# Kernel tuning notes

Hardware: AMD Instinct MI355X
Metric: run time of the kernel (lower is better)

## Reference

```python
import jax, jax.numpy as jnp
import numpy as np

EMBED = 256; G = 8; NC = 6; NL = 4; NP = 13
BS = 1; NA = 900
IMG_W, IMG_H = 704.0, 256.0
LEVEL_HW = [(64, 176), (32, 88), (16, 44), (8, 22)]


def setup_inputs() -> dict:
    key = jax.random.key(0)
    ks = jax.random.split(key, 12)
    inp = {}
    inp["instance_feature"] = jax.random.normal(ks[0], (BS, NA, EMBED), jnp.float32)
    inp["anchor_embed"] = jax.random.normal(ks[1], (BS, NA, EMBED), jnp.float32)
    # key points in normalized [0,1) cube; projection matrix maps them to pixel coords
    inp["key_points"] = jax.random.uniform(ks[2], (BS, NA, NP, 3), jnp.float32)
    for i, (h, w) in enumerate(LEVEL_HW):
        inp[f"fm{i}"] = jax.random.normal(ks[3 + i], (BS, NC, EMBED, h, w), jnp.float32)
    # intrinsics-like projection: x->x*W, y->y*H, depth ~ z+0.5, plus per-camera jitter
    base = jnp.array([[IMG_W, 0.0, 0.0, 0.0],
                      [0.0, IMG_H, 0.0, 0.0],
                      [0.0, 0.0, 1.0, 0.5],
                      [0.0, 0.0, 0.0, 1.0]], jnp.float32)
    inp["projection_mat"] = base[None, None] + 0.05 * jax.random.normal(ks[7], (BS, NC, 4, 4), jnp.float32)
    inp["image_wh"] = jnp.broadcast_to(jnp.array([IMG_W, IMG_H], jnp.float32), (BS, NC, 2))
    inp["w_weights"] = 0.02 * jax.random.normal(ks[8], (EMBED, G * NC * NL * NP), jnp.float32)
    inp["b_weights"] = jnp.zeros((G * NC * NL * NP,), jnp.float32)
    inp["w_out"] = 0.02 * jax.random.normal(ks[9], (EMBED, EMBED), jnp.float32)
    inp["b_out"] = jnp.zeros((EMBED,), jnp.float32)
    return inp


def _grid_sample(fm, grid):
    # fm: (B, C, H, W); grid: (B, A, P, 2) in [-1,1]. Bilinear, zero padding,
    # align_corners=False (torch F.grid_sample defaults). Returns (B, A, P, C).
    B, C, H, W = fm.shape
    A, P = grid.shape[1], grid.shape[2]
    gx = (grid[..., 0] + 1.0) * (W * 0.5) - 0.5
    gy = (grid[..., 1] + 1.0) * (H * 0.5) - 0.5
    x0 = jnp.floor(gx); y0 = jnp.floor(gy)
    fmf = jnp.transpose(fm.reshape(B, C, H * W), (0, 2, 1))  # (B, HW, C)

    def gather(xi, yi):
        valid = (xi >= 0) & (xi <= W - 1) & (yi >= 0) & (yi <= H - 1)
        xc = jnp.clip(xi, 0, W - 1).astype(jnp.int32)
        yc = jnp.clip(yi, 0, H - 1).astype(jnp.int32)
        idx = (yc * W + xc).reshape(B, A * P, 1)
        g = jnp.take_along_axis(fmf, idx, axis=1).reshape(B, A, P, C)
        return g * valid[..., None].astype(fm.dtype)

    wx1 = gx - x0; wx0 = 1.0 - wx1
    wy1 = gy - y0; wy0 = 1.0 - wy1
    return (gather(x0, y0) * (wx0 * wy0)[..., None]
            + gather(x0 + 1.0, y0) * (wx1 * wy0)[..., None]
            + gather(x0, y0 + 1.0) * (wx0 * wy1)[..., None]
            + gather(x0 + 1.0, y0 + 1.0) * (wx1 * wy1)[..., None])


def reference(instance_feature, anchor_embed, key_points, fm0, fm1, fm2, fm3,
              projection_mat, image_wh, w_weights, b_weights, w_out, b_out):
    bs, na = instance_feature.shape[:2]
    gd = EMBED // G
    # _get_weights: softmax over (cams*levels*pts) jointly, per group
    feat = instance_feature + anchor_embed
    w = (feat @ w_weights + b_weights).reshape(bs, na, NC * NL * NP, G)
    w = jax.nn.softmax(w, axis=2).reshape(bs, na, NC, NL, NP, G)
    # feature_sampling: project 3D key points to each camera's pixel plane
    kp_h = jnp.concatenate([key_points, jnp.ones_like(key_points[..., :1])], axis=-1)
    p2 = jnp.einsum('bcij,banj->bcani', projection_mat, kp_h)  # (bs,cams,na,pts,4)
    xy = p2[..., :2] / jnp.maximum(p2[..., 2:3], 1e-5)
    grid = (xy / image_wh[:, :, None, None]) * 2.0 - 1.0
    grid = grid.reshape(bs * NC, na, NP, 2)
    # bilinear sample every pyramid level for every camera
    feats = jnp.stack([
        _grid_sample(fm.reshape(bs * NC, EMBED, fm.shape[-2], fm.shape[-1]), grid)
        for fm in (fm0, fm1, fm2, fm3)
    ], axis=0)  # (L, bs*cams, na, pts, E)
    feats = feats.reshape(NL, bs, NC, na, NP, G, gd)
    # multi_view_level_fusion: weighted sum over cams and levels, per group
    fused = jnp.einsum('baclpg,lbcapgd->bapgd', w, feats).reshape(bs, na, NP, EMBED)
    out = fused.sum(axis=2)  # sum over key points
    return out @ w_out + b_out + instance_feature  # output_proj + residual 'add'
```

## Files before the change

kernel.cpp:

```cpp
#include <hip/hip_runtime.h>
#include <hip/hip_bf16.h>
#include <hip/hip_fp16.h>
#include <cstdint>

#define EMBED 256
#define GPS 8
#define NCAM 6
#define NLVL 4
#define NPT 13
#define NANC 900
#define NSAMP (NCAM*NLVL*NPT)
#define NWCOL (GPS*NSAMP)
#define MPAD 928
#define WSTRIDE 328
#define MAXENT 352

#define FMOFF0 0
#define FMOFF1 17301504
#define FMOFF2 21626880
#define FMOFF3 22708224
#define TALL_BYTES 22978560

typedef __attribute__((ext_vector_type(8))) short bf16x8;
typedef __attribute__((ext_vector_type(16))) float f32x16;
typedef __attribute__((ext_vector_type(2))) float v2f;

__device__ __forceinline__ ushort bf16bits(float x) {
    __hip_bfloat16 h = __float2bfloat16(x);
    return *reinterpret_cast<ushort*>(&h);
}

__global__ __launch_bounds__(256) void k_prep(
        const float* __restrict__ fm0, const float* __restrict__ fm1,
        const float* __restrict__ fm2, const float* __restrict__ fm3,
        unsigned char* __restrict__ t0, unsigned char* __restrict__ t1,
        unsigned char* __restrict__ t2, unsigned char* __restrict__ t3,
        const float* __restrict__ wlin, __hip_bfloat16* __restrict__ wt,
        const float* __restrict__ inst, const float* __restrict__ anch,
        __hip_bfloat16* __restrict__ featB,
        const float* __restrict__ kp, const float* __restrict__ proj,
        float* __restrict__ pxy) {
    __shared__ ushort lds2[128 * 64];
    int b = blockIdx.x;
    int t = threadIdx.x;
    if (b < 1404) {
        const float* in; unsigned char* outp; int HW, chunks, lb;
        if (b < 1056)      { in = fm0; outp = t0; HW = 11264; chunks = 176; lb = b; }
        else if (b < 1320) { in = fm1; outp = t1; HW = 2816;  chunks = 44;  lb = b - 1056; }
        else if (b < 1386) { in = fm2; outp = t2; HW = 704;   chunks = 11;  lb = b - 1320; }
        else               { in = fm3; outp = t3; HW = 176;   chunks = 3;   lb = b - 1386; }
        int c = lb / chunks;
        int hw0 = (lb - c * chunks) * 64;
        int q = t & 15, eg = t >> 4;
        bool vld = (hw0 + q * 4 + 3) < HW;
        const float* srcq = in + (size_t)c * EMBED * HW + hw0 + q * 4;
        float4 vals[16];
        #pragma unroll
        for (int r = 0; r < 16; r++) {
            int e = 2 * eg + (r & 1) + 32 * (r >> 1);
            vals[r] = vld ? *(const float4*)(srcq + (size_t)e * HW)
                          : make_float4(0.f, 0.f, 0.f, 0.f);
        }
        #pragma unroll
        for (int rp = 0; rp < 8; rp++) {
            int ep = eg + 16 * rp;
            int s2 = (ep >> 1) & 62;
            float4 va = vals[2 * rp], vb = vals[2 * rp + 1];
            uint p0 = (uint)__builtin_amdgcn_cvt_pk_fp8_f32(va.x, vb.x, 0, false) & 0xffff;
            uint p1 = (uint)__builtin_amdgcn_cvt_pk_fp8_f32(va.y, vb.y, 0, false) & 0xffff;
            uint p2 = (uint)__builtin_amdgcn_cvt_pk_fp8_f32(va.z, vb.z, 0, false) & 0xffff;
            uint p3 = (uint)__builtin_amdgcn_cvt_pk_fp8_f32(va.w, vb.w, 0, false) & 0xffff;
            int col01 = (q * 4) ^ s2;
            int col23 = (q * 4 + 2) ^ s2;
            *reinterpret_cast<uint*>(&lds2[ep * 64 + col01]) = p0 | (p1 << 16);
            *reinterpret_cast<uint*>(&lds2[ep * 64 + col23]) = p2 | (p3 << 16);
        }
        __syncthreads();
        ushort* outb = reinterpret_cast<ushort*>(outp) + ((size_t)c * HW + hw0) * 128;
        #pragma unroll
        for (int r = 0; r < 8; r++) {
            int flat = r * 2048 + t * 8;
            int hw = flat >> 8;
            int ep0 = (flat & 255) >> 1;
            if (hw0 + hw < HW) {
                ushort4 u;
                #pragma unroll
                for (int j = 0; j < 4; j++) {
                    int ep = ep0 + j;
                    int s2 = (ep >> 1) & 62;
                    u[j] = lds2[ep * 64 + (hw ^ s2)];
                }
                *reinterpret_cast<ushort4*>(outb + flat / 2) = u;
            }
        }
    } else if (b < 1560) {
        int b1 = b - 1404;
        int kt = b1 / 39, nt = b1 - kt * 39;
        int k0 = kt * 64, n0 = nt * 64;
        int grp = t >> 6, nn = t & 63;
        #pragma unroll
        for (int r = 0; r < 16; r++) {
            int kk = grp * 16 + r;
            lds2[kk * 65 + nn] = bf16bits(wlin[(size_t)(k0 + kk) * NWCOL + n0 + nn]);
        }
        __syncthreads();
        ushort* wtb = reinterpret_cast<ushort*>(wt);
        int kk2 = t & 63;
        #pragma unroll
        for (int r = 0; r < 16; r++) {
            int nn2 = grp * 16 + r;
            wtb[(size_t)(n0 + nn2) * EMBED + k0 + kk2] = lds2[kk2 * 65 + nn2];
        }
    } else if (b < 1785) {
        int base = (b - 1560) * 1024 + t * 4;
        float4 a = *(const float4*)&inst[base];
        float4 c = *(const float4*)&anch[base];
        ushort4 r;
        r.x = bf16bits(a.x + c.x); r.y = bf16bits(a.y + c.y);
        r.z = bf16bits(a.z + c.z); r.w = bf16bits(a.w + c.w);
        *reinterpret_cast<ushort4*>(reinterpret_cast<ushort*>(featB) + base) = r;
    } else if (b < 1792) {
        int base = 900 * EMBED + (b - 1785) * 1024 + t * 4;
        ushort4 z; z.x = z.y = z.z = z.w = 0;
        *reinterpret_cast<ushort4*>(reinterpret_cast<ushort*>(featB) + base) = z;
    } else {
        int i = (b - 1792) * 256 + t;
        if (i < NANC * NCAM * NPT) {
            int a = i / (NCAM * NPT);
            int r = i - a * (NCAM * NPT);
            int c = r / NPT;
            int p = r - c * NPT;
            const float* M = proj + c * 16;
            const float* k3 = kp + ((size_t)a * NPT + p) * 3;
            float kx = k3[0], ky = k3[1], kz = k3[2];
            float X = M[0] * kx + M[1] * ky + M[2] * kz + M[3];
            float Y = M[4] * kx + M[5] * ky + M[6] * kz + M[7];
            float Z = M[8] * kx + M[9] * ky + M[10] * kz + M[11];
            float invz = 1.f / fmaxf(Z, 1e-5f);
            pxy[(size_t)i * 2 + 0] = X * invz;
            pxy[(size_t)i * 2 + 1] = Y * invz;
        }
    }
}

#define MT 29
#define NT 78
__global__ __launch_bounds__(256) void k_gemm(const __hip_bfloat16* __restrict__ featB,
                                              const __hip_bfloat16* __restrict__ wt,
                                              const float* __restrict__ blin,
                                              float* __restrict__ logits) {
    int wv = threadIdx.x >> 6, lane = threadIdx.x & 63;
    int idx = blockIdx.x * 4 + wv;
    if (idx >= MT * NT) return;
    int mt = idx % MT, nt = idx / MT;
    int m0 = mt * 32, n0 = nt * 32;
    int l31 = lane & 31;
    int khalf = (lane >> 5) * 8;
    const short* ap = reinterpret_cast<const short*>(featB) + (size_t)(m0 + l31) * EMBED + khalf;
    const short* bp = reinterpret_cast<const short*>(wt)    + (size_t)(n0 + l31) * EMBED + khalf;
    f32x16 acc = {};
    #pragma unroll 8
    for (int ki = 0; ki < 16; ki++) {
        bf16x8 a = *reinterpret_cast<const bf16x8*>(ap + ki * 16);
        bf16x8 bb = *reinterpret_cast<const bf16x8*>(bp + ki * 16);
        acc = __builtin_amdgcn_mfma_f32_32x32x16_bf16(a, bb, acc, 0, 0, 0);
    }
    float bias = blin[n0 + l31];
    int colg = n0 + l31;
    #pragma unroll
    for (int r = 0; r < 16; r++) {
        int row = (r & 3) + 8 * (r >> 2) + 4 * (lane >> 5);
        int grow = m0 + row;
        if (grow < NANC)
            logits[(size_t)grow * NWCOL + colg] = acc[r] + bias;
    }
}

__global__ __launch_bounds__(512) void k_aggregate(const unsigned char* __restrict__ tAll,
                                                   const float* __restrict__ logits,
                                                   const float* __restrict__ pxy,
                                                   const float* __restrict__ wout,
                                                   const float* __restrict__ bout,
                                                   const float* __restrict__ inst,
                                                   float* __restrict__ out) {
    __shared__ float wT[GPS * WSTRIDE];
    __shared__ float xyS[NCAM * NPT * 2];
    __shared__ float redS[8][EMBED];
    __shared__ float pS[EMBED];
    __shared__ int4  eOff[MAXENT];
    __shared__ float4 eW[MAXENT];
    __shared__ int   eS[MAXENT];
    __shared__ int   cntS;
    int a = blockIdx.x;
    int tid = threadIdx.x;
    int wave = tid >> 6;
    int lane = tid & 63;
    if (tid == 0) cntS = 0;
    for (int j = tid; j < NWCOL; j += 512)
        wT[(j & 7) * WSTRIDE + (j >> 3)] = logits[(size_t)a * NWCOL + j];
    for (int j = tid; j < NCAM * NPT * 2; j += 512)
        xyS[j] = pxy[(size_t)a * NCAM * NPT * 2 + j];
    __syncthreads();
    {
        int g = wave;
        float m = -1e30f;
        for (int s = lane; s < NSAMP; s += 64) m = fmaxf(m, wT[g * WSTRIDE + s]);
        #pragma unroll
        for (int off = 32; off; off >>= 1) m = fmaxf(m, __shfl_xor(m, off));
        float ssum = 0.f;
        for (int s = lane; s < NSAMP; s += 64) ssum += __expf(wT[g * WSTRIDE + s] - m);
        #pragma unroll
        for (int off = 32; off; off >>= 1) ssum += __shfl_xor(ssum, off);
        float rs = 1.f / ssum;
        for (int s = lane; s < NSAMP; s += 64)
            wT[g * WSTRIDE + s] = __expf(wT[g * WSTRIDE + s] - m) * rs;
    }
    {
        bool valid = false; int4 o4; float4 w4;
        if (tid < NSAMP) {
            int c = tid / 52, rem = tid - c * 52;
            int l = rem / 13, p = rem - l * 13;
            float X = xyS[(c * NPT + p) * 2], Y = xyS[(c * NPT + p) * 2 + 1];
            int Wl = 176 >> l, Hl = 64 >> l;
            float scale = 0.25f / (float)(1 << l);
            float gx = fmaf(X, scale, -0.5f);
            float gy = fmaf(Y, scale, -0.5f);
            float x0f = floorf(gx), y0f = floorf(gy);
            float fx = gx - x0f, fy = gy - y0f;
            int x0 = (int)x0f, y0 = (int)y0f;
            int x1 = x0 + 1, y1 = y0 + 1;
            bool vx0 = (x0 >= 0) && (x0 < Wl);
            bool vx1 = (x1 >= 0) && (x1 < Wl);
            bool vy0 = (y0 >= 0) && (y0 < Hl);
            bool vy1 = (y1 >= 0) && (y1 < Hl);
            w4.x = (vx0 && vy0) ? (1.f - fx) * (1.f - fy) : 0.f;
            w4.y = (vx1 && vy0) ? fx * (1.f - fy) : 0.f;
            w4.z = (vx0 && vy1) ? (1.f - fx) * fy : 0.f;
            w4.w = (vx1 && vy1) ? fx * fy : 0.f;
            if (w4.x + w4.y + w4.z + w4.w > 0.f) {
                valid = true;
                int xc0 = min(max(x0, 0), Wl - 1), xc1 = min(max(x1, 0), Wl - 1);
                int yc0 = min(max(y0, 0), Hl - 1), yc1 = min(max(y1, 0), Hl - 1);
                const int lvlBase[4] = { FMOFF0, FMOFF1, FMOFF2, FMOFF3 };
                int cb = lvlBase[l] + c * (Wl * Hl) * EMBED;
                o4.x = cb + (yc0 * Wl + xc0) * EMBED;
                o4.y = cb + (yc0 * Wl + xc1) * EMBED;
                o4.z = cb + (yc1 * Wl + xc0) * EMBED;
                o4.w = cb + (yc1 * Wl + xc1) * EMBED;
            }
        }
        unsigned long long mask = __ballot(valid);
        int prefix = __popcll(mask & ((1ull << lane) - 1ull));
        int wcount = __popcll(mask);
        int basev = 0;
        if (lane == 0 && wcount) basev = atomicAdd(&cntS, wcount);
        basev = __shfl(basev, 0);
        if (valid) {
            int pos = basev + prefix;
            eOff[pos] = o4; eW[pos] = w4; eS[pos] = tid;
        }
    }
    __syncthreads();
    int cnt = cntS;
    int cnt_pad = (cnt + 15) & ~15;
    for (int j = cnt + tid; j < cnt_pad + 16; j += 512) {
        eOff[j] = make_int4(0, 0, 0, 0);
        eW[j] = make_float4(0.f, 0.f, 0.f, 0.f);
        eS[j] = 0;
    }
    __syncthreads();
    int e0 = lane * 4;
    int g = lane >> 3;
    float a0 = 0.f, a1 = 0.f, a2 = 0.f, a3 = 0.f;
    auto consume = [&](const float4& w, int sIdx,
                       uint c00, uint c01, uint c10, uint c11) {
        float wg = wT[g * WSTRIDE + sIdx];
        float wwx = wg * w.x, wwy = wg * w.y, wwz = wg * w.z, www = wg * w.w;
        v2f l00 = __builtin_amdgcn_cvt_pk_f32_fp8(c00, false);
        v2f h00 = __builtin_amdgcn_cvt_pk_f32_fp8(c00, true);
        v2f l01 = __builtin_amdgcn_cvt_pk_f32_fp8(c01, false);
        v2f h01 = __builtin_amdgcn_cvt_pk_f32_fp8(c01, true);
        v2f l10 = __builtin_amdgcn_cvt_pk_f32_fp8(c10, false);
        v2f h10 = __builtin_amdgcn_cvt_pk_f32_fp8(c10, true);
        v2f l11 = __builtin_amdgcn_cvt_pk_f32_fp8(c11, false);
        v2f h11 = __builtin_amdgcn_cvt_pk_f32_fp8(c11, true);
        a0 = fmaf(wwx, l00.x, fmaf(wwy, l01.x, fmaf(wwz, l10.x, fmaf(www, l11.x, a0))));
        a1 = fmaf(wwx, l00.y, fmaf(wwy, l01.y, fmaf(wwz, l10.y, fmaf(www, l11.y, a1))));
        a2 = fmaf(wwx, h00.x, fmaf(wwy, h01.x, fmaf(wwz, h10.x, fmaf(www, h11.x, a2))));
        a3 = fmaf(wwx, h00.y, fmaf(wwy, h01.y, fmaf(wwz, h10.y, fmaf(www, h11.y, a3))));
    };
    int per = cnt_pad >> 3;
    if (per > 0) {
        int idx = wave;
        int4 oA = eOff[idx]; float4 wA = eW[idx]; int sA = eS[idx];
        uint vA0 = *(const uint*)(tAll + oA.x + e0);
        uint vA1 = *(const uint*)(tAll + oA.y + e0);
        uint vA2 = *(const uint*)(tAll + oA.z + e0);
        uint vA3 = *(const uint*)(tAll + oA.w + e0);
        for (int it = 0; it < per; it += 2) {
            int j = idx + 8;
            int4 oB = eOff[j]; float4 wB = eW[j]; int sB = eS[j];
            uint vB0 = *(const uint*)(tAll + oB.x + e0);
            uint vB1 = *(const uint*)(tAll + oB.y + e0);
            uint vB2 = *(const uint*)(tAll + oB.z + e0);
            uint vB3 = *(const uint*)(tAll + oB.w + e0);
            consume(wA, sA, vA0, vA1, vA2, vA3);
            idx = j + 8;
            if (it + 2 < per) {
                oA = eOff[idx]; wA = eW[idx]; sA = eS[idx];
                vA0 = *(const uint*)(tAll + oA.x + e0);
                vA1 = *(const uint*)(tAll + oA.y + e0);
                vA2 = *(const uint*)(tAll + oA.z + e0);
                vA3 = *(const uint*)(tAll + oA.w + e0);
            }
            consume(wB, sB, vB0, vB1, vB2, vB3);
        }
    }
    redS[wave][e0 + 0] = a0; redS[wave][e0 + 1] = a1;
    redS[wave][e0 + 2] = a2; redS[wave][e0 + 3] = a3;
    __syncthreads();
    int col = tid & 255;
    int kh = tid >> 8;
    if (kh == 0) {
        float s = redS[0][col] + redS[1][col] + redS[2][col] + redS[3][col]
                + redS[4][col] + redS[5][col] + redS[6][col] + redS[7][col];
        redS[0][col] = s;
    }
    __syncthreads();
    float acc = 0.f;
    int kbase = kh * 128;
    #pragma unroll 8
    for (int k = 0; k < 128; k++)
        acc = fmaf(redS[0][kbase + k], wout[(size_t)(kbase + k) * EMBED + col], acc);
    if (kh == 1) pS[col] = acc;
    __syncthreads();
    if (kh == 0)
        out[(size_t)a * EMBED + col] = acc + pS[col] + bout[col] + inst[(size_t)a * EMBED + col];
}

extern "C" void kernel_launch(void* const* d_in, const int* in_sizes, int n_in,
                              void* d_out, int out_size, void* d_ws, size_t ws_size,
                              hipStream_t stream) {
    const float* inst = (const float*)d_in[0];
    const float* anch = (const float*)d_in[1];
    const float* kp   = (const float*)d_in[2];
    const float* fm0  = (const float*)d_in[3];
    const float* fm1  = (const float*)d_in[4];
    const float* fm2  = (const float*)d_in[5];
    const float* fm3  = (const float*)d_in[6];
    const float* proj = (const float*)d_in[7];
    const float* wlin = (const float*)d_in[9];
    const float* blin = (const float*)d_in[10];
    const float* wout = (const float*)d_in[11];
    const float* bout = (const float*)d_in[12];
    float* out = (float*)d_out;

    char* ws = (char*)d_ws;
    size_t off = 0;
    auto alloc = [&](size_t bytes) -> void* {
        void* p = ws + off;
        off = (off + bytes + 255) & ~(size_t)255;
        return p;
    };
    unsigned char* tAll = (unsigned char*)alloc((size_t)TALL_BYTES);
    unsigned char* t0 = tAll + FMOFF0;
    unsigned char* t1 = tAll + FMOFF1;
    unsigned char* t2 = tAll + FMOFF2;
    unsigned char* t3 = tAll + FMOFF3;
    __hip_bfloat16* wt    = (__hip_bfloat16*)alloc((size_t)NWCOL * EMBED * 2);
    __hip_bfloat16* featB = (__hip_bfloat16*)alloc((size_t)MPAD * EMBED * 2);
    float* logits = (float*)alloc((size_t)NANC * NWCOL * 4);
    float* pxy    = (float*)alloc((size_t)NANC * NCAM * NPT * 2 * 4);

    k_prep<<<dim3(2067), 256, 0, stream>>>(fm0, fm1, fm2, fm3, t0, t1, t2, t3,
                                           wlin, wt, inst, anch, featB, kp, proj, pxy);
    k_gemm<<<dim3((MT * NT + 3) / 4), 256, 0, stream>>>(featB, wt, blin, logits);
    k_aggregate<<<dim3(NANC), 512, 0, stream>>>(tAll, logits, pxy,
                                                wout, bout, inst, out);
}
```

Baseline: 194.9 us.

## Process two sample entries per wave with 8-byte gathers and defer softmax normalization

Each wave now splits into two 32-lane halves that handle different sample entries at the same time. Each lane gathers 8 fp8 channels with a uint2 load instead of 4, and the halves are combined with a cross-half shuffle before the block reduction. The softmax second exp pass is dropped by storing the unnormalized exponentials and applying the per-group reciprocal after the reduction. The aim is more memory-level parallelism per gather and fewer transcendental ops. In exchange each lane holds more accumulator registers, and entries are padded to a multiple of 32.

```diff
diff --git a/kernel.cpp b/kernel.cpp
--- a/kernel.cpp
+++ b/kernel.cpp
@@ -187,6 +187,7 @@
     __shared__ float xyS[NCAM * NPT * 2];
     __shared__ float redS[8][EMBED];
     __shared__ float pS[EMBED];
+    __shared__ float rsS[GPS];
     __shared__ int4  eOff[MAXENT];
     __shared__ float4 eW[MAXENT];
     __shared__ int   eS[MAXENT];
@@ -208,12 +209,14 @@
         #pragma unroll
         for (int off = 32; off; off >>= 1) m = fmaxf(m, __shfl_xor(m, off));
         float ssum = 0.f;
-        for (int s = lane; s < NSAMP; s += 64) ssum += __expf(wT[g * WSTRIDE + s] - m);
+        for (int s = lane; s < NSAMP; s += 64) {
+            float e = __expf(wT[g * WSTRIDE + s] - m);
+            wT[g * WSTRIDE + s] = e;
+            ssum += e;
+        }
         #pragma unroll
         for (int off = 32; off; off >>= 1) ssum += __shfl_xor(ssum, off);
-        float rs = 1.f / ssum;
-        for (int s = lane; s < NSAMP; s += 64)
-            wT[g * WSTRIDE + s] = __expf(wT[g * WSTRIDE + s] - m) * rs;
+        if (lane == 0) rsS[g] = 1.f / ssum;
     }
     {
         bool valid = false; int4 o4; float4 w4;
@@ -262,69 +265,85 @@
     }
     __syncthreads();
     int cnt = cntS;
-    int cnt_pad = (cnt + 15) & ~15;
-    for (int j = cnt + tid; j < cnt_pad + 16; j += 512) {
+    int cnt_pad = (cnt + 31) & ~31;
+    for (int j = cnt + tid; j < cnt_pad; j += 512) {
         eOff[j] = make_int4(0, 0, 0, 0);
         eW[j] = make_float4(0.f, 0.f, 0.f, 0.f);
         eS[j] = 0;
     }
     __syncthreads();
-    int e0 = lane * 4;
-    int g = lane >> 3;
-    float a0 = 0.f, a1 = 0.f, a2 = 0.f, a3 = 0.f;
+    int half = lane >> 5;
+    int hl = lane & 31;
+    int ch0 = hl * 8;
+    int g = hl >> 2;
+    float acc0 = 0.f, acc1 = 0.f, acc2 = 0.f, acc3 = 0.f;
+    float acc4 = 0.f, acc5 = 0.f, acc6 = 0.f, acc7 = 0.f;
     auto consume = [&](const float4& w, int sIdx,
-                       uint c00, uint c01, uint c10, uint c11) {
+                       uint2 c0, uint2 c1, uint2 c2, uint2 c3) {
         float wg = wT[g * WSTRIDE + sIdx];
-        float wwx = wg * w.x, wwy = wg * w.y, wwz = wg * w.z, www = wg * w.w;
-        v2f l00 = __builtin_amdgcn_cvt_pk_f32_fp8(c00, false);
-        v2f h00 = __builtin_amdgcn_cvt_pk_f32_fp8(c00, true);
-        v2f l01 = __builtin_amdgcn_cvt_pk_f32_fp8(c01, false);
-        v2f h01 = __builtin_amdgcn_cvt_pk_f32_fp8(c01, true);
-        v2f l10 = __builtin_amdgcn_cvt_pk_f32_fp8(c10, false);
-        v2f h10 = __builtin_amdgcn_cvt_pk_f32_fp8(c10, true);
-        v2f l11 = __builtin_amdgcn_cvt_pk_f32_fp8(c11, false);
-        v2f h11 = __builtin_amdgcn_cvt_pk_f32_fp8(c11, true);
-        a0 = fmaf(wwx, l00.x, fmaf(wwy, l01.x, fmaf(wwz, l10.x, fmaf(www, l11.x, a0))));
-        a1 = fmaf(wwx, l00.y, fmaf(wwy, l01.y, fmaf(wwz, l10.y, fmaf(www, l11.y, a1))));
-        a2 = fmaf(wwx, h00.x, fmaf(wwy, h01.x, fmaf(wwz, h10.x, fmaf(www, h11.x, a2))));
-        a3 = fmaf(wwx, h00.y, fmaf(wwy, h01.y, fmaf(wwz, h10.y, fmaf(www, h11.y, a3))));
+        float w0 = wg * w.x, w1 = wg * w.y, w2 = wg * w.z, w3 = wg * w.w;
+        v2f p;
+        p = __builtin_amdgcn_cvt_pk_f32_fp8(c0.x, false); acc0 = fmaf(w0, p.x, acc0); acc1 = fmaf(w0, p.y, acc1);
+        p = __builtin_amdgcn_cvt_pk_f32_fp8(c0.x, true);  acc2 = fmaf(w0, p.x, acc2); acc3 = fmaf(w0, p.y, acc3);
+        p = __builtin_amdgcn_cvt_pk_f32_fp8(c0.y, false); acc4 = fmaf(w0, p.x, acc4); acc5 = fmaf(w0, p.y, acc5);
+        p = __builtin_amdgcn_cvt_pk_f32_fp8(c0.y, true);  acc6 = fmaf(w0, p.x, acc6); acc7 = fmaf(w0, p.y, acc7);
+        p = __builtin_amdgcn_cvt_pk_f32_fp8(c1.x, false); acc0 = fmaf(w1, p.x, acc0); acc1 = fmaf(w1, p.y, acc1);
+        p = __builtin_amdgcn_cvt_pk_f32_fp8(c1.x, true);  acc2 = fmaf(w1, p.x, acc2); acc3 = fmaf(w1, p.y, acc3);
+        p = __builtin_amdgcn_cvt_pk_f32_fp8(c1.y, false); acc4 = fmaf(w1, p.x, acc4); acc5 = fmaf(w1, p.y, acc5);
+        p = __builtin_amdgcn_cvt_pk_f32_fp8(c1.y, true);  acc6 = fmaf(w1, p.x, acc6); acc7 = fmaf(w1, p.y, acc7);
+        p = __builtin_amdgcn_cvt_pk_f32_fp8(c2.x, false); acc0 = fmaf(w2, p.x, acc0); acc1 = fmaf(w2, p.y, acc1);
+        p = __builtin_amdgcn_cvt_pk_f32_fp8(c2.x, true);  acc2 = fmaf(w2, p.x, acc2); acc3 = fmaf(w2, p.y, acc3);
+        p = __builtin_amdgcn_cvt_pk_f32_fp8(c2.y, false); acc4 = fmaf(w2, p.x, acc4); acc5 = fmaf(w2, p.y, acc5);
+        p = __builtin_amdgcn_cvt_pk_f32_fp8(c2.y, true);  acc6 = fmaf(w2, p.x, acc6); acc7 = fmaf(w2, p.y, acc7);
+        p = __builtin_amdgcn_cvt_pk_f32_fp8(c3.x, false); acc0 = fmaf(w3, p.x, acc0); acc1 = fmaf(w3, p.y, acc1);
+        p = __builtin_amdgcn_cvt_pk_f32_fp8(c3.x, true);  acc2 = fmaf(w3, p.x, acc2); acc3 = fmaf(w3, p.y, acc3);
+        p = __builtin_amdgcn_cvt_pk_f32_fp8(c3.y, false); acc4 = fmaf(w3, p.x, acc4); acc5 = fmaf(w3, p.y, acc5);
+        p = __builtin_amdgcn_cvt_pk_f32_fp8(c3.y, true);  acc6 = fmaf(w3, p.x, acc6); acc7 = fmaf(w3, p.y, acc7);
     };
-    int per = cnt_pad >> 3;
-    if (per > 0) {
-        int idx = wave;
-        int4 oA = eOff[idx]; float4 wA = eW[idx]; int sA = eS[idx];
-        uint vA0 = *(const uint*)(tAll + oA.x + e0);
-        uint vA1 = *(const uint*)(tAll + oA.y + e0);
-        uint vA2 = *(const uint*)(tAll + oA.z + e0);
-        uint vA3 = *(const uint*)(tAll + oA.w + e0);
-        for (int it = 0; it < per; it += 2) {
-            int j = idx + 8;
-            int4 oB = eOff[j]; float4 wB = eW[j]; int sB = eS[j];
-            uint vB0 = *(const uint*)(tAll + oB.x + e0);
-            uint vB1 = *(const uint*)(tAll + oB.y + e0);
-            uint vB2 = *(const uint*)(tAll + oB.z + e0);
-            uint vB3 = *(const uint*)(tAll + oB.w + e0);
+    int steps = cnt_pad >> 4;
+    if (steps > 0) {
+        int ei = wave * 2 + half;
+        int4 oA = eOff[ei]; float4 wA = eW[ei]; int sA = eS[ei];
+        uint2 vA0 = *(const uint2*)(tAll + oA.x + ch0);
+        uint2 vA1 = *(const uint2*)(tAll + oA.y + ch0);
+        uint2 vA2 = *(const uint2*)(tAll + oA.z + ch0);
+        uint2 vA3 = *(const uint2*)(tAll + oA.w + ch0);
+        for (int it = 0; it < steps; it += 2) {
+            int ej = ei + 16;
+            int4 oB = eOff[ej]; float4 wB = eW[ej]; int sB = eS[ej];
+            uint2 vB0 = *(const uint2*)(tAll + oB.x + ch0);
+            uint2 vB1 = *(const uint2*)(tAll + oB.y + ch0);
+            uint2 vB2 = *(const uint2*)(tAll + oB.z + ch0);
+            uint2 vB3 = *(const uint2*)(tAll + oB.w + ch0);
             consume(wA, sA, vA0, vA1, vA2, vA3);
-            idx = j + 8;
-            if (it + 2 < per) {
-                oA = eOff[idx]; wA = eW[idx]; sA = eS[idx];
-                vA0 = *(const uint*)(tAll + oA.x + e0);
-                vA1 = *(const uint*)(tAll + oA.y + e0);
-                vA2 = *(const uint*)(tAll + oA.z + e0);
-                vA3 = *(const uint*)(tAll + oA.w + e0);
+            ei = ej + 16;
+            if (it + 2 < steps) {
+                oA = eOff[ei]; wA = eW[ei]; sA = eS[ei];
+                vA0 = *(const uint2*)(tAll + oA.x + ch0);
+                vA1 = *(const uint2*)(tAll + oA.y + ch0);
+                vA2 = *(const uint2*)(tAll + oA.z + ch0);
+                vA3 = *(const uint2*)(tAll + oA.w + ch0);
             }
             consume(wB, sB, vB0, vB1, vB2, vB3);
         }
     }
-    redS[wave][e0 + 0] = a0; redS[wave][e0 + 1] = a1;
-    redS[wave][e0 + 2] = a2; redS[wave][e0 + 3] = a3;
+    acc0 += __shfl_xor(acc0, 32); acc1 += __shfl_xor(acc1, 32);
+    acc2 += __shfl_xor(acc2, 32); acc3 += __shfl_xor(acc3, 32);
+    acc4 += __shfl_xor(acc4, 32); acc5 += __shfl_xor(acc5, 32);
+    acc6 += __shfl_xor(acc6, 32); acc7 += __shfl_xor(acc7, 32);
+    if (half == 0) {
+        redS[wave][ch0 + 0] = acc0; redS[wave][ch0 + 1] = acc1;
+        redS[wave][ch0 + 2] = acc2; redS[wave][ch0 + 3] = acc3;
+        redS[wave][ch0 + 4] = acc4; redS[wave][ch0 + 5] = acc5;
+        redS[wave][ch0 + 6] = acc6; redS[wave][ch0 + 7] = acc7;
+    }
     __syncthreads();
     int col = tid & 255;
     int kh = tid >> 8;
     if (kh == 0) {
         float s = redS[0][col] + redS[1][col] + redS[2][col] + redS[3][col]
                 + redS[4][col] + redS[5][col] + redS[6][col] + redS[7][col];
-        redS[0][col] = s;
+        redS[0][col] = s * rsS[col >> 5];
     }
     __syncthreads();
     float acc = 0.f;
```

After: 198.6 us. Within noise of the previous version (+1.9%).
